# Performance work log

Measured on AMD Instinct MI355X. Metric: run time of the kernel, lower is better.

Reference implementation:

```python
import jax, jax.numpy as jnp
import numpy as np

STRIDE = 1
PADDING = (1, 1, 1, 1)  # (left, right, top, bottom), as in torch F.pad for last two dims
NEG_INF = -jnp.inf


def maxplus_conv2d(x, kernel, stride=STRIDE):
    """Tropical (max-plus) conv2d, groups=1.
    x: [B, C, H, W] (already padded), kernel: [O, C, kh, kw].
    out[b,o,h,w] = max_{c,ki,kj} x[b,c,h*s+ki,w*s+kj] + kernel[o,c,ki,kj]
    """
    B, C, H, W = x.shape
    O, Cg, kh, kw = kernel.shape
    Ho = (H - kh) // stride + 1
    Wo = (W - kw) // stride + 1
    out = jnp.full((B, O, Ho, Wo), NEG_INF, dtype=x.dtype)
    # Loop over the small, fixed kernel taps (kh*kw = 9); reductions over the
    # channel axis stay fully vectorized and fuse into a single add+reduce-max.
    for ki in range(kh):
        for kj in range(kw):
            xs = x[:, :, ki:ki + Ho * stride:stride, kj:kj + Wo * stride:stride]  # [B,C,Ho,Wo]
            cand = jnp.max(xs[:, None, :, :, :] + kernel[None, :, :, ki, kj][:, :, :, None, None], axis=2)
            out = jnp.maximum(out, cand)
    return out


def setup_inputs() -> dict:
    key = jax.random.key(0)
    kx, kk = jax.random.split(key)
    x = jax.random.normal(kx, (8, 64, 64, 64), dtype=jnp.float32)
    kernel = jax.random.normal(kk, (64, 64, 3, 3), dtype=jnp.float32) * 0.1
    return {"x": x, "kernel": kernel}


def reference(x, kernel):
    left, right, top, bottom = PADDING
    # MaxPlus semifield: pad with the additive identity of max, i.e. -inf
    xp = jnp.pad(x, ((0, 0), (0, 0), (top, bottom), (left, right)), mode="constant", constant_values=NEG_INF)
    return maxplus_conv2d(xp, kernel, STRIDE)
```

## Files before the change

kernel.cpp:

```cpp
#include <hip/hip_runtime.h>

#define NEG_INF (-__builtin_huge_valf())
#define NEG_INF_BITS 0xFF800000

#define CCH   4
#define HB    4
#define ROWS  (HB + 2)
#define NROW  (CCH * ROWS)
#define XSTR  64
#define SLOTS 6

template <int CTRL>
__device__ __forceinline__ float dpp_neighbor(float v) {
    return __int_as_float(__builtin_amdgcn_update_dpp(
        (int)NEG_INF_BITS, __float_as_int(v), CTRL, 0xF, 0xF, false));
}

__device__ __forceinline__ void maxplus9(const float xv[3][6], const float* k9,
                                         float a[4]) {
#pragma unroll
    for (int wi = 0; wi < 4; ++wi) {
        float m = a[wi];
        float t0 = xv[0][wi + 0] + k9[0];
        float t1 = xv[0][wi + 1] + k9[1];
        m = fmaxf(m, fmaxf(t0, t1));
        t0 = xv[0][wi + 2] + k9[2];
        t1 = xv[1][wi + 0] + k9[3];
        m = fmaxf(m, fmaxf(t0, t1));
        t0 = xv[1][wi + 1] + k9[4];
        t1 = xv[1][wi + 2] + k9[5];
        m = fmaxf(m, fmaxf(t0, t1));
        t0 = xv[2][wi + 0] + k9[6];
        t1 = xv[2][wi + 1] + k9[7];
        m = fmaxf(m, fmaxf(t0, t1));
        m = fmaxf(m, xv[2][wi + 2] + k9[8]);
        a[wi] = m;
    }
}

__global__ __launch_bounds__(64, 2)
void maxplus_conv2d_kernel(const float* __restrict__ x,
                           const float* __restrict__ kern,
                           float* __restrict__ out) {
    __shared__ float xs[NROW * XSTR];

    const int tid = threadIdx.x;
    const int wg  = tid & 15;
    const int hr  = tid >> 4;
    const int w0  = wg << 2;

    const int h_base = blockIdx.x * HB;
    const int b      = blockIdx.y;
    const int o_base = blockIdx.z << 2;

    const float* xb = x + (size_t)b * (64 * 64 * 64);
    const float* gsrc[SLOTS];
    float*       xdst[SLOTS];
    bool         vmask[SLOTS];
#pragma unroll
    for (int k = 0; k < SLOTS; ++k) {
        int rowid = k * 4 + hr;
        int cl    = rowid / ROWS;
        int r     = rowid - cl * ROWS;
        int gh    = h_base + r - 1;
        bool v    = (unsigned)gh < 64u;
        gsrc[k]  = xb + ((size_t)cl * 64 + (v ? gh : 0)) * 64 + wg * 4;
        xdst[k]  = &xs[rowid * XSTR + wg * 4];
        vmask[k] = v;
    }

    float acc[4][4];
#pragma unroll
    for (int oo = 0; oo < 4; ++oo)
#pragma unroll
        for (int wi = 0; wi < 4; ++wi)
            acc[oo][wi] = NEG_INF;

    float4 R[SLOTS];
#pragma unroll
    for (int k = 0; k < SLOTS; ++k) R[k] = *(const float4*)gsrc[k];

#pragma unroll 1
    for (int cc = 0; cc < 64; cc += CCH) {
        __syncthreads();

#pragma unroll
        for (int k = 0; k < SLOTS; ++k) {
            float4 v = R[k];
            if (!vmask[k]) v = make_float4(NEG_INF, NEG_INF, NEG_INF, NEG_INF);
            *(float4*)xdst[k] = v;
        }

        __syncthreads();

        if (cc + CCH < 64) {
#pragma unroll
            for (int k = 0; k < SLOTS; ++k) {
                gsrc[k] += CCH * 64 * 64;
                R[k] = *(const float4*)gsrc[k];
            }
        }

#pragma unroll
        for (int op = 0; op < 2; ++op) {
            float kv[CCH][2][9];
#pragma unroll
            for (int cl = 0; cl < CCH; ++cl)
#pragma unroll
                for (int oo = 0; oo < 2; ++oo) {
                    const float* kp =
                        kern + ((size_t)(o_base + op * 2 + oo) * 64 + (cc + cl)) * 9;
#pragma unroll
                    for (int t = 0; t < 9; ++t) kv[cl][oo][t] = kp[t];
                }

#pragma unroll
            for (int cl = 0; cl < CCH; ++cl) {
                float xv[3][6];
#pragma unroll
                for (int r = 0; r < 3; ++r) {
                    const int rowid = cl * ROWS + hr + r;
                    float4 m = *(const float4*)(&xs[rowid * XSTR + w0]);
                    xv[r][0] = dpp_neighbor<0x111>(m.w);
                    xv[r][1] = m.x; xv[r][2] = m.y; xv[r][3] = m.z; xv[r][4] = m.w;
                    xv[r][5] = dpp_neighbor<0x101>(m.x);
                }
                maxplus9(xv, kv[cl][0], acc[op * 2 + 0]);
                maxplus9(xv, kv[cl][1], acc[op * 2 + 1]);
            }
        }
    }

    const int h = h_base + hr;
#pragma unroll
    for (int oo = 0; oo < 4; ++oo) {
        float4 v = make_float4(acc[oo][0], acc[oo][1], acc[oo][2], acc[oo][3]);
        *(float4*)(out + ((((size_t)b * 64 + (o_base + oo)) * 64 + h) * 64 + w0)) = v;
    }
}

extern "C" void kernel_launch(void* const* d_in, const int* in_sizes, int n_in,
                              void* d_out, int out_size, void* d_ws, size_t ws_size,
                              hipStream_t stream) {
    const float* x    = (const float*)d_in[0];
    const float* kern = (const float*)d_in[1];
    float* out = (float*)d_out;

    dim3 grid(16, 8, 16);
    dim3 block(64);
    maxplus_conv2d_kernel<<<grid, block, 0, stream>>>(x, kern, out);
}
```

Before: 121.2 us.

## Drop LDS staging, load input rows directly from global with two outputs per block

Removes the shared-memory tile, the register prefetch and both barriers, so each thread now reads its three input rows per channel straight from global memory (relying on L1/L2 for the vertical halo reuse). Output channels per block drop from four to two, which doubles the grid, and launch bounds are raised to allow more waves per SIMD. This trades LDS traffic and synchronisation for redundant global/cache loads and less reuse of each input load across output channels.

```diff
diff --git a/kernel.cpp b/kernel.cpp
--- a/kernel.cpp
+++ b/kernel.cpp
@@ -2,13 +2,6 @@
 
 #define NEG_INF (-__builtin_huge_valf())
 #define NEG_INF_BITS 0xFF800000
-
-#define CCH   4
-#define HB    4
-#define ROWS  (HB + 2)
-#define NROW  (CCH * ROWS)
-#define XSTR  64
-#define SLOTS 6
 
 template <int CTRL>
 __device__ __forceinline__ float dpp_neighbor(float v) {
@@ -38,102 +31,78 @@
     }
 }
 
-__global__ __launch_bounds__(64, 2)
+__global__ __launch_bounds__(64, 4)
 void maxplus_conv2d_kernel(const float* __restrict__ x,
                            const float* __restrict__ kern,
                            float* __restrict__ out) {
-    __shared__ float xs[NROW * XSTR];
-
     const int tid = threadIdx.x;
     const int wg  = tid & 15;
     const int hr  = tid >> 4;
     const int w0  = wg << 2;
 
-    const int h_base = blockIdx.x * HB;
+    const int h_base = blockIdx.x * 4;
     const int b      = blockIdx.y;
-    const int o_base = blockIdx.z << 2;
+    const int o_base = blockIdx.z << 1;
 
     const float* xb = x + (size_t)b * (64 * 64 * 64);
-    const float* gsrc[SLOTS];
-    float*       xdst[SLOTS];
-    bool         vmask[SLOTS];
+
+    int  off[3];
+    bool rv[3];
 #pragma unroll
-    for (int k = 0; k < SLOTS; ++k) {
-        int rowid = k * 4 + hr;
-        int cl    = rowid / ROWS;
-        int r     = rowid - cl * ROWS;
-        int gh    = h_base + r - 1;
-        bool v    = (unsigned)gh < 64u;
-        gsrc[k]  = xb + ((size_t)cl * 64 + (v ? gh : 0)) * 64 + wg * 4;
-        xdst[k]  = &xs[rowid * XSTR + wg * 4];
-        vmask[k] = v;
+    for (int r = 0; r < 3; ++r) {
+        int gh = h_base + hr - 1 + r;
+        rv[r]  = (unsigned)gh < 64u;
+        off[r] = (rv[r] ? gh : 0) * 64 + w0;
     }
 
-    float acc[4][4];
+    float acc[2][4];
 #pragma unroll
-    for (int oo = 0; oo < 4; ++oo)
+    for (int oo = 0; oo < 2; ++oo)
 #pragma unroll
         for (int wi = 0; wi < 4; ++wi)
             acc[oo][wi] = NEG_INF;
 
-    float4 R[SLOTS];
-#pragma unroll
-    for (int k = 0; k < SLOTS; ++k) R[k] = *(const float4*)gsrc[k];
+    const float* kp0 = kern + (size_t)(o_base + 0) * (64 * 9);
+    const float* kp1 = kern + (size_t)(o_base + 1) * (64 * 9);
 
 #pragma unroll 1
-    for (int cc = 0; cc < 64; cc += CCH) {
-        __syncthreads();
+    for (int cc = 0; cc < 64; cc += 4) {
+        float kv[4][2][9];
+#pragma unroll
+        for (int cl = 0; cl < 4; ++cl)
+#pragma unroll
+            for (int t = 0; t < 9; ++t) {
+                kv[cl][0][t] = kp0[(cc + cl) * 9 + t];
+                kv[cl][1][t] = kp1[(cc + cl) * 9 + t];
+            }
+
+        float4 mm[4][3];
+#pragma unroll
+        for (int cl = 0; cl < 4; ++cl)
+#pragma unroll
+            for (int r = 0; r < 3; ++r)
+                mm[cl][r] = *(const float4*)(xb + ((cc + cl) * 4096 + off[r]));
 
 #pragma unroll
-        for (int k = 0; k < SLOTS; ++k) {
-            float4 v = R[k];
-            if (!vmask[k]) v = make_float4(NEG_INF, NEG_INF, NEG_INF, NEG_INF);
-            *(float4*)xdst[k] = v;
-        }
-
-        __syncthreads();
-
-        if (cc + CCH < 64) {
+        for (int cl = 0; cl < 4; ++cl) {
+            float xv[3][6];
 #pragma unroll
-            for (int k = 0; k < SLOTS; ++k) {
-                gsrc[k] += CCH * 64 * 64;
-                R[k] = *(const float4*)gsrc[k];
+            for (int r = 0; r < 3; ++r) {
+                float4 m = mm[cl][r];
+                if (r != 1 && !rv[r])
+                    m = make_float4(NEG_INF, NEG_INF, NEG_INF, NEG_INF);
+                xv[r][0] = dpp_neighbor<0x111>(m.w);
+                xv[r][1] = m.x; xv[r][2] = m.y; xv[r][3] = m.z; xv[r][4] = m.w;
+                xv[r][5] = dpp_neighbor<0x101>(m.x);
             }
-        }
-
-#pragma unroll
-        for (int op = 0; op < 2; ++op) {
-            float kv[CCH][2][9];
-#pragma unroll
-            for (int cl = 0; cl < CCH; ++cl)
-#pragma unroll
-                for (int oo = 0; oo < 2; ++oo) {
-                    const float* kp =
-                        kern + ((size_t)(o_base + op * 2 + oo) * 64 + (cc + cl)) * 9;
-#pragma unroll
-                    for (int t = 0; t < 9; ++t) kv[cl][oo][t] = kp[t];
-                }
-
-#pragma unroll
-            for (int cl = 0; cl < CCH; ++cl) {
-                float xv[3][6];
-#pragma unroll
-                for (int r = 0; r < 3; ++r) {
-                    const int rowid = cl * ROWS + hr + r;
-                    float4 m = *(const float4*)(&xs[rowid * XSTR + w0]);
-                    xv[r][0] = dpp_neighbor<0x111>(m.w);
-                    xv[r][1] = m.x; xv[r][2] = m.y; xv[r][3] = m.z; xv[r][4] = m.w;
-                    xv[r][5] = dpp_neighbor<0x101>(m.x);
-                }
-                maxplus9(xv, kv[cl][0], acc[op * 2 + 0]);
-                maxplus9(xv, kv[cl][1], acc[op * 2 + 1]);
-            }
+            maxplus9(xv, kv[cl][0], acc[0]);
+            maxplus9(xv, kv[cl][1], acc[1]);
         }
     }
 
     const int h = h_base + hr;
 #pragma unroll
-    for (int oo = 0; oo < 4; ++oo) {
+    for (int oo = 0; oo < 2; ++oo) {
         float4 v = make_float4(acc[oo][0], acc[oo][1], acc[oo][2], acc[oo][3]);
         *(float4*)(out + ((((size_t)b * 64 + (o_base + oo)) * 64 + h) * 64 + w0)) = v;
     }
@@ -146,7 +115,7 @@
     const float* kern = (const float*)d_in[1];
     float* out = (float*)d_out;
 
-    dim3 grid(16, 8, 16);
+    dim3 grid(16, 8, 32);
     dim3 block(64);
     maxplus_conv2d_kernel<<<grid, block, 0, stream>>>(x, kern, out);
 }
```

Result: no change. 121.1 us (-0.2%).
